# Kernel optimization log

Hardware: AMD Instinct MI355X
Metric: run time of the kernel (lower is better)

Reference implementation:

```python
import jax, jax.numpy as jnp
import numpy as np

N, NH, G, SEG, RATIO = 500000, 128, 10000, 25, 2
P = G * SEG            # 250000 pos samples
PN = P * RATIO         # 500000 neg samples


def setup_inputs() -> dict:
    key = jax.random.key(0)
    k1, k2, k3, k4, k5, k6 = jax.random.split(key, 6)
    return {
        "embedding": jax.random.normal(k1, (N, NH), jnp.float32),
        "embedding_": jax.random.normal(k2, (N, NH), jnp.float32),
        "grid_sizes": jnp.full((G,), SEG, dtype=jnp.int64 if jax.config.jax_enable_x64 else jnp.int32),
        "pos_samples": jax.random.randint(k3, (P,), 0, N),
        "neg_samples": jax.random.randint(k4, (PN,), 0, N),
        "Wi": jax.random.normal(k5, (NH, NH), jnp.float32) * (1.0 / np.sqrt(NH)),
        "bi": jnp.zeros((NH,), jnp.float32),
        "Wk": jax.random.normal(k6, (NH, NH), jnp.float32) * (1.0 / np.sqrt(NH)),  # Bilinear weight [1,nh,nh] squeezed
        "bk": jnp.zeros((1,), jnp.float32),
    }


def reference(embedding, embedding_, grid_sizes, pos_samples, neg_samples, Wi, bi, Wk, bk):
    Pl = pos_samples.shape[0]
    Gl = grid_sizes.shape[0]
    ratio = neg_samples.shape[0] // Pl  # static int

    # segment ids: grid index repeated grid_sizes[i] times (sum == P)
    seg_ids = jnp.repeat(jnp.arange(Gl), grid_sizes, total_repeat_length=Pl)

    # f_i on embedding_ , gather pos, segment-mean per grid
    emb_ = embedding_ @ Wi.T + bi                      # [N, nh]
    pos_e_ = emb_[pos_samples]                         # [P, nh]
    seg_sum = jax.ops.segment_sum(pos_e_, seg_ids, num_segments=Gl)
    grid_embed = seg_sum / grid_sizes[:, None].astype(seg_sum.dtype)  # [G, nh]

    # f_i on embedding, gather pos/neg samples
    emb = embedding @ Wi.T + bi
    pos_embed = emb[pos_samples]                       # [P, nh]
    neg_embed = emb[neg_samples]                       # [P*ratio, nh]

    # broadcast grid embedding back to per-sample rows
    pos_grid = grid_embed[seg_ids]                     # [P, nh]
    neg_seg_ids = jnp.repeat(jnp.arange(Gl), grid_sizes * ratio,
                             total_repeat_length=Pl * ratio)
    neg_grid = grid_embed[neg_seg_ids]                 # [P*ratio, nh]

    # bilinear score: x1 W x2 + b (out features = 1, squeezed)
    pos_logits = jnp.einsum('nd,de,ne->n', pos_embed, Wk, pos_grid) + bk[0]
    neg_logits = jnp.einsum('nd,de,ne->n', neg_embed, Wk, neg_grid) + bk[0]
    return jnp.concatenate((pos_logits, neg_logits))
```

## Files before the change

kernel.cpp:

```cpp
#include <hip/hip_runtime.h>

#define NH 128

__global__ void setup1_kernel(const int* __restrict__ gs, int* __restrict__ c, int G,
                              const float* __restrict__ Wk, const float* __restrict__ Wi,
                              const float* __restrict__ bi,
                              float* __restrict__ A, float* __restrict__ u) {
    if (blockIdx.x == 0) {
        __shared__ int part[1024];
        int t = threadIdx.x;
        int chunk = (G + 1023) >> 10;
        int b = t * chunk;
        int e = min(b + chunk, G);
        int s = 0;
        for (int i = b; i < e; ++i) s += gs[i];
        part[t] = s;
        __syncthreads();
        for (int off = 1; off < 1024; off <<= 1) {
            int val = (t >= off) ? part[t - off] : 0;
            __syncthreads();
            part[t] += val;
            __syncthreads();
        }
        int excl = (t == 0) ? 0 : part[t - 1];
        for (int i = b; i < e; ++i) { c[i] = excl; excl += gs[i]; }
        if (t == 1023) c[G] = part[1023];
    } else {
        int tid = (blockIdx.x - 1) * 1024 + threadIdx.x;
        int e = tid >> 7, d = tid & (NH - 1);
        float acc = 0.f;
        for (int f = 0; f < NH; ++f) acc += Wk[e * NH + f] * Wi[f * NH + d];
        A[e * NH + d] = acc;
        if (tid < NH) {
            float s = 0.f;
            for (int f = 0; f < NH; ++f) s += Wk[tid * NH + f] * bi[f];
            u[tid] = s;
        }
    }
}

__global__ void matB_kernel(const float* __restrict__ Wi, const float* __restrict__ bi,
                            const float* __restrict__ bk,
                            const float* __restrict__ A, const float* __restrict__ u,
                            float* __restrict__ Bt, float* __restrict__ v,
                            float* __restrict__ w, float* __restrict__ s0) {
    int tid = blockIdx.x * blockDim.x + threadIdx.x;
    int i = tid & (NH - 1);
    int j = tid >> 7;
    float acc = 0.f;
    for (int e = 0; e < NH; ++e) acc += Wi[e * NH + i] * A[e * NH + j];
    Bt[j * NH + i] = acc;
    if (tid < NH) {
        float s = 0.f;
        for (int e = 0; e < NH; ++e) s += Wi[e * NH + tid] * u[e];
        v[tid] = s;
    } else if (tid < 2 * NH) {
        int jj = tid - NH;
        float s = 0.f;
        for (int e = 0; e < NH; ++e) s += bi[e] * A[e * NH + jj];
        w[jj] = s;
    }
    if (tid == 0) {
        float s = 0.f;
        for (int e = 0; e < NH; ++e) s += bi[e] * u[e];
        s0[0] = s + bk[0];
    }
}

#define MCH 8
__global__ __launch_bounds__(256, 8)
void seg_mean_kernel(const float* __restrict__ emb_, const int* __restrict__ pos,
                     const int* __restrict__ c, float* __restrict__ M,
                     int* __restrict__ segid, int G) {
    int wave  = (blockIdx.x * blockDim.x + threadIdx.x) >> 6;
    int lane  = threadIdx.x & 63;
    int nwave = (gridDim.x * blockDim.x) >> 6;
    for (int g = wave; g < G; g += nwave) {
        int pb = c[g], pe = c[g + 1];
        int np = pe - pb;
        float2 acc = make_float2(0.f, 0.f);
        for (int r0 = 0; r0 < np; r0 += 64) {
            int nr = min(64, np - r0);
            int idxv = 0;
            if (lane < nr) {
                idxv = pos[pb + r0 + lane];
                segid[pb + r0 + lane] = g;
            }
            int r = 0;
            for (; r + MCH <= nr; r += MCH) {
                float2 a[MCH];
#pragma unroll
                for (int j = 0; j < MCH; ++j) {
                    int row = __shfl(idxv, r + j, 64);
                    a[j] = ((const float2*)(emb_ + (size_t)row * NH))[lane];
                }
#pragma unroll
                for (int j = 0; j < MCH; ++j) { acc.x += a[j].x; acc.y += a[j].y; }
            }
            for (; r < nr; ++r) {
                int row = __shfl(idxv, r, 64);
                float2 a = ((const float2*)(emb_ + (size_t)row * NH))[lane];
                acc.x += a.x; acc.y += a.y;
            }
        }
        float cnt = (float)max(np, 1);
        ((float2*)(M + (size_t)g * NH))[lane] = make_float2(acc.x / cnt, acc.y / cnt);
    }
}

#define SPB 8
__global__ void q_kernel(const float* __restrict__ M, const float* __restrict__ Bt,
                         const float* __restrict__ v, const float* __restrict__ w,
                         const float* __restrict__ s0,
                         float* __restrict__ Q, float* __restrict__ C2, int G) {
    __shared__ float m[SPB][NH];
    __shared__ float red[SPB][2];
    int d = threadIdx.x;
    int g0 = blockIdx.x * SPB;
    int ns = min(SPB, G - g0);
    for (int s = 0; s < SPB; ++s)
        m[s][d] = (s < ns) ? M[(size_t)(g0 + s) * NH + d] : 0.f;
    __syncthreads();

    float q[SPB];
#pragma unroll
    for (int s = 0; s < SPB; ++s) q[s] = 0.f;
    for (int f = 0; f < NH; ++f) {
        float bt = Bt[f * NH + d];
#pragma unroll
        for (int s = 0; s < SPB; ++s) q[s] += bt * m[s][f];
    }
    float vd = v[d], wd = w[d], s00 = s0[0];
    for (int s = 0; s < ns; ++s)
        Q[(size_t)(g0 + s) * NH + d] = q[s] + vd;

    int lane = d & 63, wv = d >> 6;
    for (int s = 0; s < SPB; ++s) {
        float tval = wd * m[s][d];
        for (int off = 32; off; off >>= 1) tval += __shfl_xor(tval, off);
        if (lane == 0) red[s][wv] = tval;
    }
    __syncthreads();
    if (d < SPB && d < ns) C2[g0 + d] = red[d][0] + red[d][1] + s00;
}

#define U 4
__global__ __launch_bounds__(256, 6)
void logits_kernel(const float* __restrict__ emb, const int* __restrict__ pos,
                   const int* __restrict__ neg, const int* __restrict__ segid,
                   const float* __restrict__ Q, const float* __restrict__ C2,
                   float* __restrict__ out, int P, int PN,
                   unsigned long long magic) {
    int tot = P + PN;
    int gid  = (blockIdx.x * blockDim.x + threadIdx.x) >> 5;
    int lane = threadIdx.x & 31;
    int ngrp = (gridDim.x * blockDim.x) >> 5;
    long long stride = (long long)ngrp * U;

    for (long long base = (long long)gid * U; base < tot; base += stride) {
        int kk[U], row[U], sid[U];
#pragma unroll
        for (int j = 0; j < U; ++j) {
            int k = (int)base + j;
            int k2 = (k < tot) ? k : (tot - 1);
            kk[j] = k2;
            if (k2 < P) {
                row[j] = pos[k2];
                sid[j] = segid[k2];
            } else {
                int jn = k2 - P;
                row[j] = neg[jn];
                int jp = (int)(((unsigned long long)(unsigned)jn * magic) >> 42);
                sid[j] = segid[jp];
            }
        }
        float4 a[U], q[U];
        float c2v[U];
#pragma unroll
        for (int j = 0; j < U; ++j) {
            a[j]   = ((const float4*)(emb + (size_t)row[j] * NH))[lane];
            q[j]   = ((const float4*)(Q   + (size_t)sid[j] * NH))[lane];
            c2v[j] = C2[sid[j]];
        }
#pragma unroll
        for (int j = 0; j < U; ++j) {
            float val = a[j].x * q[j].x + a[j].y * q[j].y
                      + a[j].z * q[j].z + a[j].w * q[j].w;
#pragma unroll
            for (int off = 16; off; off >>= 1) val += __shfl_xor(val, off, 32);
            if (lane == 0 && base + j < tot) out[kk[j]] = val + c2v[j];
        }
    }
}

extern "C" void kernel_launch(void* const* d_in, const int* in_sizes, int n_in,
                              void* d_out, int out_size, void* d_ws, size_t ws_size,
                              hipStream_t stream) {
    const float* embedding  = (const float*)d_in[0];
    const float* embedding_ = (const float*)d_in[1];
    const int*   grid_sizes = (const int*)d_in[2];
    const int*   pos        = (const int*)d_in[3];
    const int*   neg        = (const int*)d_in[4];
    const float* Wi         = (const float*)d_in[5];
    const float* bi         = (const float*)d_in[6];
    const float* Wk         = (const float*)d_in[7];
    const float* bk         = (const float*)d_in[8];

    int G = in_sizes[2];
    int P = in_sizes[3];
    int PN = in_sizes[4];
    int ratio = (P > 0) ? (PN / P) : 1;
    if (ratio < 1) ratio = 1;
    unsigned long long magic = (((unsigned long long)1 << 42) + ratio - 1) / (unsigned long long)ratio;

    char* ws = (char*)d_ws;
    size_t off = 0;
    auto alloc = [&](size_t bytes) {
        void* p = ws + off;
        off += (bytes + 255) & ~(size_t)255;
        return p;
    };
    int*   c     = (int*)  alloc((size_t)(G + 1) * sizeof(int));
    float* A     = (float*)alloc(NH * NH * sizeof(float));
    float* u     = (float*)alloc(NH * sizeof(float));
    float* Bt    = (float*)alloc(NH * NH * sizeof(float));
    float* v     = (float*)alloc(NH * sizeof(float));
    float* w     = (float*)alloc(NH * sizeof(float));
    float* s0    = (float*)alloc(sizeof(float));
    float* M     = (float*)alloc((size_t)G * NH * sizeof(float));
    float* Q     = (float*)alloc((size_t)G * NH * sizeof(float));
    float* C2    = (float*)alloc((size_t)G * sizeof(float));
    int*   segid = (int*)  alloc((size_t)P * sizeof(int));
    (void)ws_size; (void)n_in; (void)out_size;

    hipLaunchKernelGGL(setup1_kernel, dim3(1 + (NH * NH) / 1024), dim3(1024), 0, stream,
                       grid_sizes, c, G, Wk, Wi, bi, A, u);
    hipLaunchKernelGGL(matB_kernel, dim3((NH * NH) / 256), dim3(256), 0, stream,
                       Wi, bi, bk, A, u, Bt, v, w, s0);
    int smblocks = (G + 3) / 4;
    hipLaunchKernelGGL(seg_mean_kernel, dim3(smblocks), dim3(256), 0, stream,
                       embedding_, pos, c, M, segid, G);
    hipLaunchKernelGGL(q_kernel, dim3((G + SPB - 1) / SPB), dim3(NH), 0, stream,
                       M, Bt, v, w, s0, Q, C2, G);
    hipLaunchKernelGGL(logits_kernel, dim3(2048), dim3(256), 0, stream,
                       embedding, pos, neg, segid, Q, C2, (float*)d_out, P, PN, magic);
}
```

Measured before the change: 528.5 us.

## Fuse weight-setup kernels and merge segment-mean with Q projection

Merges the two weight-precompute kernels into one launch in which a single 1024-thread block computes A and u into shared memory and then Bt, v, w and s0. The segment-mean kernel is fused with the Q/C2 projection, so each wave multiplies its mean row by Bt using shuffles and writes Q and C2 directly. This drops two launches and the M intermediate round-trip through global memory. The cost is that the full 128x128x128 weight product now runs serially in one block, and each wave re-reads Bt per segment.

```diff
diff --git a/kernel.cpp b/kernel.cpp
--- a/kernel.cpp
+++ b/kernel.cpp
@@ -2,10 +2,12 @@
 
 #define NH 128
 
-__global__ void setup1_kernel(const int* __restrict__ gs, int* __restrict__ c, int G,
-                              const float* __restrict__ Wk, const float* __restrict__ Wi,
-                              const float* __restrict__ bi,
-                              float* __restrict__ A, float* __restrict__ u) {
+__global__ __launch_bounds__(1024)
+void setup_kernel(const int* __restrict__ gs, int* __restrict__ c, int G,
+                  const float* __restrict__ Wk, const float* __restrict__ Wi,
+                  const float* __restrict__ bi, const float* __restrict__ bk,
+                  float* __restrict__ Bt, float* __restrict__ v,
+                  float* __restrict__ w, float* __restrict__ s0) {
     if (blockIdx.x == 0) {
         __shared__ int part[1024];
         int t = threadIdx.x;
@@ -26,58 +28,60 @@
         for (int i = b; i < e; ++i) { c[i] = excl; excl += gs[i]; }
         if (t == 1023) c[G] = part[1023];
     } else {
-        int tid = (blockIdx.x - 1) * 1024 + threadIdx.x;
-        int e = tid >> 7, d = tid & (NH - 1);
-        float acc = 0.f;
-        for (int f = 0; f < NH; ++f) acc += Wk[e * NH + f] * Wi[f * NH + d];
-        A[e * NH + d] = acc;
-        if (tid < NH) {
-            float s = 0.f;
-            for (int f = 0; f < NH; ++f) s += Wk[tid * NH + f] * bi[f];
-            u[tid] = s;
+        __shared__ float A_s[NH * NH];
+        __shared__ float u_s[NH];
+        int t = threadIdx.x;
+        for (int idx = t; idx < NH * NH; idx += 1024) {
+            int e = idx >> 7, d = idx & (NH - 1);
+            float acc = 0.f;
+            for (int f = 0; f < NH; ++f) acc += Wk[e * NH + f] * Wi[f * NH + d];
+            A_s[idx] = acc;
+        }
+        if (t < NH) {
+            float s = 0.f;
+            for (int f = 0; f < NH; ++f) s += Wk[t * NH + f] * bi[f];
+            u_s[t] = s;
+        }
+        __syncthreads();
+        for (int idx = t; idx < NH * NH; idx += 1024) {
+            int i = idx & (NH - 1), j = idx >> 7;
+            float acc = 0.f;
+            for (int e = 0; e < NH; ++e) acc += Wi[e * NH + i] * A_s[e * NH + j];
+            Bt[j * NH + i] = acc;
+        }
+        if (t < NH) {
+            float s = 0.f;
+            for (int e = 0; e < NH; ++e) s += Wi[e * NH + t] * u_s[e];
+            v[t] = s;
+        } else if (t < 2 * NH) {
+            int jj = t - NH;
+            float s = 0.f;
+            for (int e = 0; e < NH; ++e) s += bi[e] * A_s[e * NH + jj];
+            w[jj] = s;
+        } else if (t == 2 * NH) {
+            float s = 0.f;
+            for (int e = 0; e < NH; ++e) s += bi[e] * u_s[e];
+            s0[0] = s + bk[0];
         }
     }
 }
 
-__global__ void matB_kernel(const float* __restrict__ Wi, const float* __restrict__ bi,
-                            const float* __restrict__ bk,
-                            const float* __restrict__ A, const float* __restrict__ u,
-                            float* __restrict__ Bt, float* __restrict__ v,
-                            float* __restrict__ w, float* __restrict__ s0) {
-    int tid = blockIdx.x * blockDim.x + threadIdx.x;
-    int i = tid & (NH - 1);
-    int j = tid >> 7;
-    float acc = 0.f;
-    for (int e = 0; e < NH; ++e) acc += Wi[e * NH + i] * A[e * NH + j];
-    Bt[j * NH + i] = acc;
-    if (tid < NH) {
-        float s = 0.f;
-        for (int e = 0; e < NH; ++e) s += Wi[e * NH + tid] * u[e];
-        v[tid] = s;
-    } else if (tid < 2 * NH) {
-        int jj = tid - NH;
-        float s = 0.f;
-        for (int e = 0; e < NH; ++e) s += bi[e] * A[e * NH + jj];
-        w[jj] = s;
-    }
-    if (tid == 0) {
-        float s = 0.f;
-        for (int e = 0; e < NH; ++e) s += bi[e] * u[e];
-        s0[0] = s + bk[0];
-    }
-}
-
 #define MCH 8
-__global__ __launch_bounds__(256, 8)
-void seg_mean_kernel(const float* __restrict__ emb_, const int* __restrict__ pos,
-                     const int* __restrict__ c, float* __restrict__ M,
-                     int* __restrict__ segid, int G) {
+__global__ __launch_bounds__(256)
+void segq_kernel(const float* __restrict__ emb_, const int* __restrict__ pos,
+                 const int* __restrict__ c, const float* __restrict__ Bt,
+                 const float* __restrict__ v, const float* __restrict__ w,
+                 const float* __restrict__ s0, float* __restrict__ Q,
+                 float* __restrict__ C2, int* __restrict__ segid, int G) {
     int wave  = (blockIdx.x * blockDim.x + threadIdx.x) >> 6;
     int lane  = threadIdx.x & 63;
     int nwave = (gridDim.x * blockDim.x) >> 6;
+    const float2* Bt2 = (const float2*)Bt;
+
     for (int g = wave; g < G; g += nwave) {
         int pb = c[g], pe = c[g + 1];
         int np = pe - pb;
+
         float2 acc = make_float2(0.f, 0.f);
         for (int r0 = 0; r0 < np; r0 += 64) {
             int nr = min(64, np - r0);
@@ -104,44 +108,27 @@
             }
         }
         float cnt = (float)max(np, 1);
-        ((float2*)(M + (size_t)g * NH))[lane] = make_float2(acc.x / cnt, acc.y / cnt);
+        float mx = acc.x / cnt, my = acc.y / cnt;
+
+        float qx = 0.f, qy = 0.f;
+#pragma unroll 8
+        for (int j = 0; j < 64; ++j) {
+            float mf0 = __shfl(mx, j, 64);
+            float mf1 = __shfl(my, j, 64);
+            float2 b0 = Bt2[(2 * j)     * 64 + lane];
+            float2 b1 = Bt2[(2 * j + 1) * 64 + lane];
+            qx += b0.x * mf0 + b1.x * mf1;
+            qy += b0.y * mf0 + b1.y * mf1;
+        }
+        float2 vv = ((const float2*)v)[lane];
+        ((float2*)(Q + (size_t)g * NH))[lane] = make_float2(qx + vv.x, qy + vv.y);
+
+        float2 ww = ((const float2*)w)[lane];
+        float cv = ww.x * mx + ww.y * my;
+#pragma unroll
+        for (int off = 32; off; off >>= 1) cv += __shfl_xor(cv, off, 64);
+        if (lane == 0) C2[g] = cv + s0[0];
     }
-}
-
-#define SPB 8
-__global__ void q_kernel(const float* __restrict__ M, const float* __restrict__ Bt,
-                         const float* __restrict__ v, const float* __restrict__ w,
-                         const float* __restrict__ s0,
-                         float* __restrict__ Q, float* __restrict__ C2, int G) {
-    __shared__ float m[SPB][NH];
-    __shared__ float red[SPB][2];
-    int d = threadIdx.x;
-    int g0 = blockIdx.x * SPB;
-    int ns = min(SPB, G - g0);
-    for (int s = 0; s < SPB; ++s)
-        m[s][d] = (s < ns) ? M[(size_t)(g0 + s) * NH + d] : 0.f;
-    __syncthreads();
-
-    float q[SPB];
-#pragma unroll
-    for (int s = 0; s < SPB; ++s) q[s] = 0.f;
-    for (int f = 0; f < NH; ++f) {
-        float bt = Bt[f * NH + d];
-#pragma unroll
-        for (int s = 0; s < SPB; ++s) q[s] += bt * m[s][f];
-    }
-    float vd = v[d], wd = w[d], s00 = s0[0];
-    for (int s = 0; s < ns; ++s)
-        Q[(size_t)(g0 + s) * NH + d] = q[s] + vd;
-
-    int lane = d & 63, wv = d >> 6;
-    for (int s = 0; s < SPB; ++s) {
-        float tval = wd * m[s][d];
-        for (int off = 32; off; off >>= 1) tval += __shfl_xor(tval, off);
-        if (lane == 0) red[s][wv] = tval;
-    }
-    __syncthreads();
-    if (d < SPB && d < ns) C2[g0 + d] = red[d][0] + red[d][1] + s00;
 }
 
 #define U 4
@@ -221,27 +208,20 @@
         return p;
     };
     int*   c     = (int*)  alloc((size_t)(G + 1) * sizeof(int));
-    float* A     = (float*)alloc(NH * NH * sizeof(float));
-    float* u     = (float*)alloc(NH * sizeof(float));
     float* Bt    = (float*)alloc(NH * NH * sizeof(float));
     float* v     = (float*)alloc(NH * sizeof(float));
     float* w     = (float*)alloc(NH * sizeof(float));
     float* s0    = (float*)alloc(sizeof(float));
-    float* M     = (float*)alloc((size_t)G * NH * sizeof(float));
     float* Q     = (float*)alloc((size_t)G * NH * sizeof(float));
     float* C2    = (float*)alloc((size_t)G * sizeof(float));
     int*   segid = (int*)  alloc((size_t)P * sizeof(int));
     (void)ws_size; (void)n_in; (void)out_size;
 
-    hipLaunchKernelGGL(setup1_kernel, dim3(1 + (NH * NH) / 1024), dim3(1024), 0, stream,
-                       grid_sizes, c, G, Wk, Wi, bi, A, u);
-    hipLaunchKernelGGL(matB_kernel, dim3((NH * NH) / 256), dim3(256), 0, stream,
-                       Wi, bi, bk, A, u, Bt, v, w, s0);
-    int smblocks = (G + 3) / 4;
-    hipLaunchKernelGGL(seg_mean_kernel, dim3(smblocks), dim3(256), 0, stream,
-                       embedding_, pos, c, M, segid, G);
-    hipLaunchKernelGGL(q_kernel, dim3((G + SPB - 1) / SPB), dim3(NH), 0, stream,
-                       M, Bt, v, w, s0, Q, C2, G);
+    hipLaunchKernelGGL(setup_kernel, dim3(2), dim3(1024), 0, stream,
+                       grid_sizes, c, G, Wk, Wi, bi, bk, Bt, v, w, s0);
+    int sqblocks = (G + 3) / 4;
+    hipLaunchKernelGGL(segq_kernel, dim3(sqblocks), dim3(256), 0, stream,
+                       embedding_, pos, c, Bt, v, w, s0, Q, C2, segid, G);
     hipLaunchKernelGGL(logits_kernel, dim3(2048), dim3(256), 0, stream,
                        embedding, pos, neg, segid, Q, C2, (float*)d_out, P, PN, magic);
 }
```

Measured after the change: 699.5 us. +32.4%, slower.
